# Kernel optimization log

Measured on AMD Instinct MI355X. Metric: run time of the kernel, lower is better.

## Reference

```python
import jax, jax.numpy as jnp
import numpy as np

B, S, D, H = 4, 2048, 1024, 16
DK = D // H


def setup_inputs() -> dict:
    key = jax.random.key(0)
    ks = jax.random.split(key, 12)
    def xavier(k, shape):
        fan_in, fan_out = shape[1], shape[0]
        limit = (6.0 / (fan_in + fan_out)) ** 0.5
        return jax.random.uniform(k, shape, jnp.float32, -limit, limit)
    inp = {
        "q": jax.random.normal(ks[0], (B, S, D), jnp.float32),
        "k": jax.random.normal(ks[1], (B, S, D), jnp.float32),
        "v": jax.random.normal(ks[2], (B, S, D), jnp.float32),
        "mask": jnp.ones((1, 1, S, S), jnp.int32),
        "Wq": xavier(ks[3], (D, D)), "bq": jnp.zeros((D,), jnp.float32),
        "Wk": xavier(ks[4], (D, D)), "bk": jnp.zeros((D,), jnp.float32),
        "Wv": xavier(ks[5], (D, D)), "bv": jnp.zeros((D,), jnp.float32),
        "Wo": xavier(ks[6], (D, D)), "bo": jnp.zeros((D,), jnp.float32),
        "ln_g": jnp.ones((D,), jnp.float32),
        "ln_b": jnp.zeros((D,), jnp.float32),
    }
    return inp


def _split_heads(x):
    b, s, _ = x.shape
    return x.reshape(b, s, H, DK).transpose(0, 2, 1, 3)  # [B,H,S,dk]


def reference(q, k, v, mask, Wq, bq, Wk, bk, Wv, bv, Wo, bo, ln_g, ln_b):
    residual = q
    qh = _split_heads(q @ Wq.T + bq)
    kh = _split_heads(k @ Wk.T + bk)
    vh = _split_heads(v @ Wv.T + bv)
    scale = jnp.sqrt(jnp.asarray(DK, qh.dtype))
    scores = jnp.einsum("bhqd,bhkd->bhqk", qh, kh) / scale  # [B,H,S,S]
    scores = jnp.where(mask == 0, jnp.asarray(-1e9, scores.dtype), scores)
    m = jnp.max(scores, axis=-1, keepdims=True)
    e = jnp.exp(scores - m) * mask.astype(scores.dtype)
    probs = e / (jnp.sum(e, axis=-1, keepdims=True) + 1e-9)
    attn = jnp.einsum("bhqk,bhkd->bhqd", probs, vh)
    attn = attn.transpose(0, 2, 1, 3).reshape(q.shape[0], -1, D)
    out = attn @ Wo.T + bo
    x = out + residual
    mu = jnp.mean(x, axis=-1, keepdims=True)
    var = jnp.mean((x - mu) ** 2, axis=-1, keepdims=True)
    return (x - mu) / jnp.sqrt(var + 1e-5) * ln_g + ln_b
```

## Files before the change

### kernel.cpp

```cpp
#include <hip/hip_runtime.h>
#include <hip/hip_bf16.h>
#include <stdint.h>

#define B_  4
#define S_  2048
#define D_  1024
#define H_  16
#define DK_ 64
#define M_  (B_ * S_)

typedef __bf16 bf16x8 __attribute__((ext_vector_type(8)));
typedef float  f32x4  __attribute__((ext_vector_type(4)));

__device__ __forceinline__ void gl_lds16(const void* g, void* l) {
  __builtin_amdgcn_global_load_lds(
      (const __attribute__((address_space(1))) void*)g,
      (__attribute__((address_space(3))) void*)l, 16, 0, 0);
}

__global__ __launch_bounds__(256)
void cvt_kernel(const float* __restrict__ src, __bf16* __restrict__ dst) {
  const int i = blockIdx.x * 256 + threadIdx.x;
  const float4 a = ((const float4*)src)[i * 2];
  const float4 b = ((const float4*)src)[i * 2 + 1];
  bf16x8 o;
  o[0] = (__bf16)a.x; o[1] = (__bf16)a.y; o[2] = (__bf16)a.z; o[3] = (__bf16)a.w;
  o[4] = (__bf16)b.x; o[5] = (__bf16)b.y; o[6] = (__bf16)b.z; o[7] = (__bf16)b.w;
  ((bf16x8*)dst)[i] = o;
}

__global__ __launch_bounds__(256)
void cvt_w_kernel(const float* __restrict__ s0, const float* __restrict__ s1,
                  const float* __restrict__ s2, const float* __restrict__ s3,
                  __bf16* __restrict__ dst) {
  const float* s = blockIdx.y == 0 ? s0 : blockIdx.y == 1 ? s1
                  : blockIdx.y == 2 ? s2 : s3;
  __bf16* d = dst + (long)blockIdx.y * (D_ * D_);
  const int i = blockIdx.x * 256 + threadIdx.x;
  const float4 a = ((const float4*)s)[i * 2];
  const float4 b = ((const float4*)s)[i * 2 + 1];
  bf16x8 o;
  o[0] = (__bf16)a.x; o[1] = (__bf16)a.y; o[2] = (__bf16)a.z; o[3] = (__bf16)a.w;
  o[4] = (__bf16)b.x; o[5] = (__bf16)b.y; o[6] = (__bf16)b.z; o[7] = (__bf16)b.w;
  ((bf16x8*)d)[i] = o;
}

template <int MODE>
__global__ __launch_bounds__(256)
void gemm_bt_kernel(const __bf16* __restrict__ A,
                    const __bf16* __restrict__ W,
                    const float* __restrict__ bias,
                    __bf16* __restrict__ outh,
                    float* __restrict__ outf,
                    const float* __restrict__ resid,
                    float scale) {
  __shared__ __bf16 Asm[128 * 32];
  __shared__ __bf16 Bsm[128 * 32];
  const int tid  = threadIdx.x;
  const int lane = tid & 63;
  const int wave = tid >> 6;
  const int wm = (wave >> 1) * 64, wn = (wave & 1) * 64;
  const int m0 = blockIdx.y * 128, n0 = blockIdx.x * 128;
  const int lr = lane & 15, lq = lane >> 4;

  const int r0 = tid >> 2;
  const int c0 = (tid & 3) * 8;
  const __bf16* Ap0 = A + (long)(m0 + r0) * D_ + c0;
  const __bf16* Ap1 = A + (long)(m0 + 64 + r0) * D_ + c0;
  const __bf16* Wp0 = W + (long)(n0 + r0) * D_ + c0;
  const __bf16* Wp1 = W + (long)(n0 + 64 + r0) * D_ + c0;
  __bf16* AsmW0 = &Asm[tid * 8];
  __bf16* AsmW1 = &Asm[(256 + tid) * 8];
  __bf16* BsmW0 = &Bsm[tid * 8];
  __bf16* BsmW1 = &Bsm[(256 + tid) * 8];

  f32x4 acc[4][4] = {};

  for (int k0 = 0; k0 < D_; k0 += 32) {
    gl_lds16(Ap0 + k0, AsmW0);
    gl_lds16(Ap1 + k0, AsmW1);
    gl_lds16(Wp0 + k0, BsmW0);
    gl_lds16(Wp1 + k0, BsmW1);
    __syncthreads();
    bf16x8 af[4], bf[4];
#pragma unroll
    for (int i = 0; i < 4; i++)
      af[i] = *(const bf16x8*)&Asm[(wm + i * 16 + lr) * 32 + lq * 8];
#pragma unroll
    for (int j = 0; j < 4; j++)
      bf[j] = *(const bf16x8*)&Bsm[(wn + j * 16 + lr) * 32 + lq * 8];
#pragma unroll
    for (int i = 0; i < 4; i++)
#pragma unroll
      for (int j = 0; j < 4; j++)
        acc[i][j] = __builtin_amdgcn_mfma_f32_16x16x32_bf16(af[i], bf[j],
                                                            acc[i][j], 0, 0, 0);
    __syncthreads();
  }

#pragma unroll
  for (int j = 0; j < 4; j++) {
    const int n = n0 + wn + j * 16 + lr;
    const float bb = bias[n];
#pragma unroll
    for (int i = 0; i < 4; i++) {
      const int mbase = m0 + wm + i * 16 + lq * 4;
#pragma unroll
      for (int r = 0; r < 4; r++) {
        const int m = mbase + r;
        float v = acc[i][j][r];
        if (MODE == 0) {
          v = (v + bb) * scale;
          const int b = m >> 11, s = m & (S_ - 1);
          const int h = n >> 6, dk = n & 63;
          outh[(((long)(b * H_ + h) * S_ + s)) * DK_ + dk] = (__bf16)v;
        } else {
          outf[(long)m * D_ + n] = v + bb + resid[(long)m * D_ + n];
        }
      }
    }
  }
}

__global__ __launch_bounds__(256)
void transpose_v_kernel(const __bf16* __restrict__ Vh, __bf16* __restrict__ Vt) {
  __shared__ __bf16 tile[64 * 80];
  const int tid = threadIdx.x;
  const int bh = blockIdx.y;
  const int s0 = blockIdx.x * 64;
#pragma unroll
  for (int c = 0; c < 2; c++) {
    const int idx = c * 256 + tid;
    const int sl = idx >> 3, ch = idx & 7;
    *(uint4*)&tile[sl * 80 + ch * 8] =
        *(const uint4*)&Vh[((long)bh * S_ + s0 + sl) * DK_ + ch * 8];
  }
  __syncthreads();
#pragma unroll
  for (int c = 0; c < 2; c++) {
    const int idx = c * 256 + tid;
    const int dk = idx >> 3, ch = idx & 7;
    __bf16 tmp[8];
#pragma unroll
    for (int j = 0; j < 8; j++) tmp[j] = tile[(ch * 8 + j) * 80 + dk];
    *(uint4*)&Vt[((long)bh * DK_ + dk) * S_ + s0 + ch * 8] = *(const uint4*)tmp;
  }
}

__global__ __launch_bounds__(256)
void attn_kernel(const __bf16* __restrict__ Qh,
                 const __bf16* __restrict__ Kh,
                 const __bf16* __restrict__ Vt,
                 __bf16* __restrict__ ctx) {
  __shared__ __bf16 Ksm[64 * 64];
  __shared__ __bf16 Vsm[64 * 64];
  __shared__ __bf16 Psm[4 * 32 * 72];
  const int tid = threadIdx.x, lane = tid & 63, wave = tid >> 6;
  const int lr = lane & 15, lq = lane >> 4;
  const int bh = blockIdx.z * H_ + blockIdx.y;
  const int q0 = blockIdx.x * 128 + wave * 32;
  const long base = (long)bh * S_ * DK_;
  __bf16* Pw = &Psm[wave * 32 * 72];

  bf16x8 qf[2][2];
#pragma unroll
  for (int qg = 0; qg < 2; qg++)
#pragma unroll
    for (int c = 0; c < 2; c++)
      qf[qg][c] = *(const bf16x8*)
          &Qh[base + (long)(q0 + qg * 16 + lr) * DK_ + c * 32 + lq * 8];

  f32x4 o[2][4] = {};
  float lsum[2] = {0.f, 0.f};

  for (int kt = 0; kt < S_ / 64; kt++) {
    const int k0 = kt * 64;
#pragma unroll
    for (int c = 0; c < 2; c++) {
      const int idx = c * 256 + tid;
      const int row = idx >> 3, ch = (idx & 7) * 8;
      gl_lds16(&Kh[base + (long)(k0 + row) * DK_ + ch], &Ksm[idx * 8]);
      gl_lds16(&Vt[base + (long)row * S_ + k0 + ch], &Vsm[idx * 8]);
    }
    __syncthreads();

    f32x4 sc[2][4];
#pragma unroll
    for (int nt = 0; nt < 4; nt++) {
      bf16x8 kf0 = *(const bf16x8*)&Ksm[(nt * 16 + lr) * 64 + lq * 8];
      bf16x8 kf1 = *(const bf16x8*)&Ksm[(nt * 16 + lr) * 64 + 32 + lq * 8];
#pragma unroll
      for (int qg = 0; qg < 2; qg++) {
        f32x4 z = {};
        z = __builtin_amdgcn_mfma_f32_16x16x32_bf16(kf0, qf[qg][0], z, 0, 0, 0);
        z = __builtin_amdgcn_mfma_f32_16x16x32_bf16(kf1, qf[qg][1], z, 0, 0, 0);
        sc[qg][nt] = z;
      }
    }

#pragma unroll
    for (int qg = 0; qg < 2; qg++) {
      float rs = 0.f;
      __bf16* prow = &Pw[(qg * 16 + lr) * 72 + lq * 4];
#pragma unroll
      for (int nt = 0; nt < 4; nt++) {
        union { __bf16 h[4]; uint2 u; } pk;
#pragma unroll
        for (int r = 0; r < 4; r++) {
          const float p = __builtin_amdgcn_exp2f(sc[qg][nt][r]);
          rs += p;
          pk.h[r] = (__bf16)p;
        }
        *(uint2*)&prow[nt * 16] = pk.u;
      }
      lsum[qg] += rs;
    }

    bf16x8 pf[2][2];
#pragma unroll
    for (int qg = 0; qg < 2; qg++) {
      pf[qg][0] = *(const bf16x8*)&Pw[(qg * 16 + lr) * 72 + lq * 8];
      pf[qg][1] = *(const bf16x8*)&Pw[(qg * 16 + lr) * 72 + 32 + lq * 8];
    }
#pragma unroll
    for (int d = 0; d < 4; d++) {
      bf16x8 vf0 = *(const bf16x8*)&Vsm[(d * 16 + lr) * 64 + lq * 8];
      bf16x8 vf1 = *(const bf16x8*)&Vsm[(d * 16 + lr) * 64 + 32 + lq * 8];
#pragma unroll
      for (int qg = 0; qg < 2; qg++) {
        o[qg][d] = __builtin_amdgcn_mfma_f32_16x16x32_bf16(pf[qg][0], vf0,
                                                           o[qg][d], 0, 0, 0);
        o[qg][d] = __builtin_amdgcn_mfma_f32_16x16x32_bf16(pf[qg][1], vf1,
                                                           o[qg][d], 0, 0, 0);
      }
    }
    __syncthreads();
  }

  const int b = blockIdx.z, h = blockIdx.y;
#pragma unroll
  for (int qg = 0; qg < 2; qg++) {
    float t = lsum[qg];
    t += __shfl_xor(t, 16);
    t += __shfl_xor(t, 32);
#pragma unroll
    for (int r = 0; r < 4; r++) {
      const float ls = __shfl(t, (lane & 48) | (lq * 4 + r));
      const float inv = 1.f / (ls + 1e-9f);
      const int srow = q0 + qg * 16 + lq * 4 + r;
#pragma unroll
      for (int d = 0; d < 4; d++)
        ctx[((long)b * S_ + srow) * D_ + h * DK_ + d * 16 + lr] =
            (__bf16)(o[qg][d][r] * inv);
    }
  }
}

__global__ __launch_bounds__(256)
void ln_kernel(float* __restrict__ x, const float* __restrict__ g,
               const float* __restrict__ bta) {
  const int lane = threadIdx.x & 63, wave = threadIdx.x >> 6;
  const int row = blockIdx.x * 4 + wave;
  float* xp = x + (long)row * D_;
  float v[16], sum = 0.f, ssq = 0.f;
#pragma unroll
  for (int c = 0; c < 4; c++) {
    const float4 t = *(const float4*)&xp[lane * 16 + c * 4];
    v[c * 4 + 0] = t.x; v[c * 4 + 1] = t.y; v[c * 4 + 2] = t.z; v[c * 4 + 3] = t.w;
  }
#pragma unroll
  for (int j = 0; j < 16; j++) {
    sum += v[j];
    ssq += v[j] * v[j];
  }
#pragma unroll
  for (int off = 1; off < 64; off <<= 1) {
    sum += __shfl_xor(sum, off);
    ssq += __shfl_xor(ssq, off);
  }
  const float mu = sum * (1.f / 1024.f);
  const float var = ssq * (1.f / 1024.f) - mu * mu;
  const float rstd = rsqrtf(var + 1e-5f);
#pragma unroll
  for (int c = 0; c < 4; c++) {
    float4 t;
    const int cbase = lane * 16 + c * 4;
    t.x = (v[c * 4 + 0] - mu) * rstd * g[cbase + 0] + bta[cbase + 0];
    t.y = (v[c * 4 + 1] - mu) * rstd * g[cbase + 1] + bta[cbase + 1];
    t.z = (v[c * 4 + 2] - mu) * rstd * g[cbase + 2] + bta[cbase + 2];
    t.w = (v[c * 4 + 3] - mu) * rstd * g[cbase + 3] + bta[cbase + 3];
    *(float4*)&xp[cbase] = t;
  }
}

extern "C" void kernel_launch(void* const* d_in, const int* in_sizes, int n_in,
                              void* d_out, int out_size, void* d_ws,
                              size_t ws_size, hipStream_t stream) {
  const float* q   = (const float*)d_in[0];
  const float* k   = (const float*)d_in[1];
  const float* v   = (const float*)d_in[2];
  const float* Wq  = (const float*)d_in[4];
  const float* bq  = (const float*)d_in[5];
  const float* Wk  = (const float*)d_in[6];
  const float* bk  = (const float*)d_in[7];
  const float* Wv  = (const float*)d_in[8];
  const float* bv  = (const float*)d_in[9];
  const float* Wo  = (const float*)d_in[10];
  const float* bo  = (const float*)d_in[11];
  const float* lng = (const float*)d_in[12];
  const float* lnb = (const float*)d_in[13];
  float* out = (float*)d_out;
  __bf16* ws = (__bf16*)d_ws;

  const long SZ = (long)M_ * D_;
  const long WN = (long)D_ * D_;
  __bf16* cbuf = ws;
  __bf16* Wb   = ws + SZ;
  __bf16* Qh   = ws + SZ + 4 * WN;
  __bf16* Kh   = Qh + SZ;
  __bf16* Vh   = Qh + 2 * SZ;
  __bf16* Vt   = Qh + 3 * SZ;
  __bf16* ctx  = cbuf;

  const int CG = (int)(SZ / 8 / 256);
  const dim3 gg(D_ / 128, M_ / 128);
  const float qscale = 0.125f * 1.44269504f;

  cvt_w_kernel<<<dim3(WN / 8 / 256, 4), 256, 0, stream>>>(Wq, Wk, Wv, Wo, Wb);

  cvt_kernel<<<CG, 256, 0, stream>>>(q, cbuf);
  gemm_bt_kernel<0><<<gg, 256, 0, stream>>>(cbuf, Wb + 0 * WN, bq, Qh, nullptr,
                                            nullptr, qscale);
  cvt_kernel<<<CG, 256, 0, stream>>>(k, cbuf);
  gemm_bt_kernel<0><<<gg, 256, 0, stream>>>(cbuf, Wb + 1 * WN, bk, Kh, nullptr,
                                            nullptr, 1.0f);
  cvt_kernel<<<CG, 256, 0, stream>>>(v, cbuf);
  gemm_bt_kernel<0><<<gg, 256, 0, stream>>>(cbuf, Wb + 2 * WN, bv, Vh, nullptr,
                                            nullptr, 1.0f);
  transpose_v_kernel<<<dim3(S_ / 64, B_ * H_), 256, 0, stream>>>(Vh, Vt);
  attn_kernel<<<dim3(S_ / 128, H_, B_), 256, 0, stream>>>(Qh, Kh, Vt, ctx);
  gemm_bt_kernel<1><<<gg, 256, 0, stream>>>(ctx, Wb + 3 * WN, bo, nullptr, out,
                                            q, 1.0f);
  ln_kernel<<<M_ / 4, 256, 0, stream>>>(out, lng, lnb);
}
```

Baseline: 439.1 us.

## Fuse fp32-to-bf16 conversion into batched QKV projection and swizzle LDS layouts

Removes the three separate activation conversion kernels by loading fp32 inputs directly in the projection GEMM, converting in registers and writing bf16 into LDS. The Q, K and V projections are merged into one launch using a z grid dimension. XOR swizzles are applied to the GEMM and attention LDS tiles to reduce bank conflicts. The trade-off is that A-tile loads now go through registers instead of direct global-to-LDS copies and read twice as many bytes as fp32, which may expose more load latency.

```diff
diff --git a/kernel.cpp b/kernel.cpp
--- a/kernel.cpp
+++ b/kernel.cpp
@@ -18,15 +18,11 @@
       (__attribute__((address_space(3))) void*)l, 16, 0, 0);
 }
 
-__global__ __launch_bounds__(256)
-void cvt_kernel(const float* __restrict__ src, __bf16* __restrict__ dst) {
-  const int i = blockIdx.x * 256 + threadIdx.x;
-  const float4 a = ((const float4*)src)[i * 2];
-  const float4 b = ((const float4*)src)[i * 2 + 1];
+__device__ __forceinline__ bf16x8 pack8(float4 a, float4 b) {
   bf16x8 o;
   o[0] = (__bf16)a.x; o[1] = (__bf16)a.y; o[2] = (__bf16)a.z; o[3] = (__bf16)a.w;
   o[4] = (__bf16)b.x; o[5] = (__bf16)b.y; o[6] = (__bf16)b.z; o[7] = (__bf16)b.w;
-  ((bf16x8*)dst)[i] = o;
+  return o;
 }
 
 __global__ __launch_bounds__(256)
@@ -37,23 +33,107 @@
                   : blockIdx.y == 2 ? s2 : s3;
   __bf16* d = dst + (long)blockIdx.y * (D_ * D_);
   const int i = blockIdx.x * 256 + threadIdx.x;
-  const float4 a = ((const float4*)s)[i * 2];
-  const float4 b = ((const float4*)s)[i * 2 + 1];
-  bf16x8 o;
-  o[0] = (__bf16)a.x; o[1] = (__bf16)a.y; o[2] = (__bf16)a.z; o[3] = (__bf16)a.w;
-  o[4] = (__bf16)b.x; o[5] = (__bf16)b.y; o[6] = (__bf16)b.z; o[7] = (__bf16)b.w;
-  ((bf16x8*)d)[i] = o;
-}
-
-template <int MODE>
-__global__ __launch_bounds__(256)
-void gemm_bt_kernel(const __bf16* __restrict__ A,
-                    const __bf16* __restrict__ W,
-                    const float* __restrict__ bias,
-                    __bf16* __restrict__ outh,
-                    float* __restrict__ outf,
-                    const float* __restrict__ resid,
-                    float scale) {
+  ((bf16x8*)d)[i] =
+      pack8(((const float4*)s)[i * 2], ((const float4*)s)[i * 2 + 1]);
+}
+
+__global__ __launch_bounds__(256)
+void proj_qkv_kernel(const float* __restrict__ qin, const float* __restrict__ kin,
+                     const float* __restrict__ vin, const __bf16* __restrict__ Wb,
+                     const float* __restrict__ bq, const float* __restrict__ bk,
+                     const float* __restrict__ bv, __bf16* __restrict__ Qh,
+                     float qscale) {
+  __shared__ __bf16 Asm[128 * 32];
+  __shared__ __bf16 Bsm[128 * 32];
+  const int z = blockIdx.z;
+  const float* A = z == 0 ? qin : z == 1 ? kin : vin;
+  const __bf16* W = Wb + (long)z * (D_ * D_);
+  const float* bias = z == 0 ? bq : z == 1 ? bk : bv;
+  const float scale = z == 0 ? qscale : 1.0f;
+  __bf16* dst = Qh + (long)z * ((long)M_ * D_);
+
+  const int tid  = threadIdx.x;
+  const int lane = tid & 63;
+  const int wave = tid >> 6;
+  const int wm = (wave >> 1) * 64, wn = (wave & 1) * 64;
+  const int m0 = blockIdx.y * 128, n0 = blockIdx.x * 128;
+  const int lr = lane & 15, lq = lane >> 4;
+
+  const int ar  = tid >> 1;
+  const int acg = (tid & 1) * 2;
+  const int asw = (ar >> 1) & 3;
+  const float* Aptr = A + (long)(m0 + ar) * D_ + acg * 8;
+  __bf16* AsmW0 = &Asm[ar * 32 + ((acg    ) ^ asw) * 8];
+  __bf16* AsmW1 = &Asm[ar * 32 + ((acg + 1) ^ asw) * 8];
+
+  const int r0  = tid >> 2;
+  const int bcg = ((tid & 3) ^ ((r0 >> 1) & 3)) * 8;
+  const __bf16* Wp0 = W + (long)(n0 + r0) * D_ + bcg;
+  const __bf16* Wp1 = W + (long)(n0 + 64 + r0) * D_ + bcg;
+  __bf16* BsmW0 = &Bsm[tid * 8];
+  __bf16* BsmW1 = &Bsm[(256 + tid) * 8];
+
+  int aoff[4], boff[4];
+#pragma unroll
+  for (int i = 0; i < 4; i++) {
+    const int row = wm + i * 16 + lr;
+    aoff[i] = row * 32 + ((lq ^ ((row >> 1) & 3)) * 8);
+  }
+#pragma unroll
+  for (int j = 0; j < 4; j++) {
+    const int row = wn + j * 16 + lr;
+    boff[j] = row * 32 + ((lq ^ ((row >> 1) & 3)) * 8);
+  }
+
+  f32x4 acc[4][4] = {};
+
+  for (int k0 = 0; k0 < D_; k0 += 32) {
+    const float4 f0 = *(const float4*)(Aptr + k0);
+    const float4 f1 = *(const float4*)(Aptr + k0 + 4);
+    const float4 f2 = *(const float4*)(Aptr + k0 + 8);
+    const float4 f3 = *(const float4*)(Aptr + k0 + 12);
+    gl_lds16(Wp0 + k0, BsmW0);
+    gl_lds16(Wp1 + k0, BsmW1);
+    *(bf16x8*)AsmW0 = pack8(f0, f1);
+    *(bf16x8*)AsmW1 = pack8(f2, f3);
+    __syncthreads();
+    bf16x8 af[4], bf[4];
+#pragma unroll
+    for (int i = 0; i < 4; i++) af[i] = *(const bf16x8*)&Asm[aoff[i]];
+#pragma unroll
+    for (int j = 0; j < 4; j++) bf[j] = *(const bf16x8*)&Bsm[boff[j]];
+#pragma unroll
+    for (int i = 0; i < 4; i++)
+#pragma unroll
+      for (int j = 0; j < 4; j++)
+        acc[i][j] = __builtin_amdgcn_mfma_f32_16x16x32_bf16(af[i], bf[j],
+                                                            acc[i][j], 0, 0, 0);
+    __syncthreads();
+  }
+
+#pragma unroll
+  for (int j = 0; j < 4; j++) {
+    const int n = n0 + wn + j * 16 + lr;
+    const float bb = bias[n];
+#pragma unroll
+    for (int i = 0; i < 4; i++) {
+      const int mbase = m0 + wm + i * 16 + lq * 4;
+#pragma unroll
+      for (int r = 0; r < 4; r++) {
+        const int m = mbase + r;
+        const float v = (acc[i][j][r] + bb) * scale;
+        const int b = m >> 11, s = m & (S_ - 1);
+        const int h = n >> 6, dk = n & 63;
+        dst[(((long)(b * H_ + h) * S_ + s)) * DK_ + dk] = (__bf16)v;
+      }
+    }
+  }
+}
+
+__global__ __launch_bounds__(256)
+void gemm_out_kernel(const __bf16* __restrict__ A, const __bf16* __restrict__ W,
+                     const float* __restrict__ bias, float* __restrict__ outf,
+                     const float* __restrict__ resid) {
   __shared__ __bf16 Asm[128 * 32];
   __shared__ __bf16 Bsm[128 * 32];
   const int tid  = threadIdx.x;
@@ -64,15 +144,27 @@
   const int lr = lane & 15, lq = lane >> 4;
 
   const int r0 = tid >> 2;
-  const int c0 = (tid & 3) * 8;
-  const __bf16* Ap0 = A + (long)(m0 + r0) * D_ + c0;
-  const __bf16* Ap1 = A + (long)(m0 + 64 + r0) * D_ + c0;
-  const __bf16* Wp0 = W + (long)(n0 + r0) * D_ + c0;
-  const __bf16* Wp1 = W + (long)(n0 + 64 + r0) * D_ + c0;
+  const int cg = ((tid & 3) ^ ((r0 >> 1) & 3)) * 8;
+  const __bf16* Ap0 = A + (long)(m0 + r0) * D_ + cg;
+  const __bf16* Ap1 = A + (long)(m0 + 64 + r0) * D_ + cg;
+  const __bf16* Wp0 = W + (long)(n0 + r0) * D_ + cg;
+  const __bf16* Wp1 = W + (long)(n0 + 64 + r0) * D_ + cg;
   __bf16* AsmW0 = &Asm[tid * 8];
   __bf16* AsmW1 = &Asm[(256 + tid) * 8];
   __bf16* BsmW0 = &Bsm[tid * 8];
   __bf16* BsmW1 = &Bsm[(256 + tid) * 8];
+
+  int aoff[4], boff[4];
+#pragma unroll
+  for (int i = 0; i < 4; i++) {
+    const int row = wm + i * 16 + lr;
+    aoff[i] = row * 32 + ((lq ^ ((row >> 1) & 3)) * 8);
+  }
+#pragma unroll
+  for (int j = 0; j < 4; j++) {
+    const int row = wn + j * 16 + lr;
+    boff[j] = row * 32 + ((lq ^ ((row >> 1) & 3)) * 8);
+  }
 
   f32x4 acc[4][4] = {};
 
@@ -84,11 +176,9 @@
     __syncthreads();
     bf16x8 af[4], bf[4];
 #pragma unroll
-    for (int i = 0; i < 4; i++)
-      af[i] = *(const bf16x8*)&Asm[(wm + i * 16 + lr) * 32 + lq * 8];
-#pragma unroll
-    for (int j = 0; j < 4; j++)
-      bf[j] = *(const bf16x8*)&Bsm[(wn + j * 16 + lr) * 32 + lq * 8];
+    for (int i = 0; i < 4; i++) af[i] = *(const bf16x8*)&Asm[aoff[i]];
+#pragma unroll
+    for (int j = 0; j < 4; j++) bf[j] = *(const bf16x8*)&Bsm[boff[j]];
 #pragma unroll
     for (int i = 0; i < 4; i++)
 #pragma unroll
@@ -108,15 +198,7 @@
 #pragma unroll
       for (int r = 0; r < 4; r++) {
         const int m = mbase + r;
-        float v = acc[i][j][r];
-        if (MODE == 0) {
-          v = (v + bb) * scale;
-          const int b = m >> 11, s = m & (S_ - 1);
-          const int h = n >> 6, dk = n & 63;
-          outh[(((long)(b * H_ + h) * S_ + s)) * DK_ + dk] = (__bf16)v;
-        } else {
-          outf[(long)m * D_ + n] = v + bb + resid[(long)m * D_ + n];
-        }
+        outf[(long)m * D_ + n] = acc[i][j][r] + bb + resid[(long)m * D_ + n];
       }
     }
   }
@@ -170,6 +252,10 @@
       qf[qg][c] = *(const bf16x8*)
           &Qh[base + (long)(q0 + qg * 16 + lr) * DK_ + c * 32 + lq * 8];
 
+  const int cl0 = (lq ^ (lr & 7)) * 8;
+  const int cl1 = ((lq + 4) ^ (lr & 7)) * 8;
+  const int rbase = lr * 64;
+
   f32x4 o[2][4] = {};
   float lsum[2] = {0.f, 0.f};
 
@@ -178,17 +264,18 @@
 #pragma unroll
     for (int c = 0; c < 2; c++) {
       const int idx = c * 256 + tid;
-      const int row = idx >> 3, ch = (idx & 7) * 8;
-      gl_lds16(&Kh[base + (long)(k0 + row) * DK_ + ch], &Ksm[idx * 8]);
-      gl_lds16(&Vt[base + (long)row * S_ + k0 + ch], &Vsm[idx * 8]);
+      const int row = idx >> 3;
+      const int cgl = ((idx & 7) ^ (row & 7)) * 8;
+      gl_lds16(&Kh[base + (long)(k0 + row) * DK_ + cgl], &Ksm[idx * 8]);
+      gl_lds16(&Vt[base + (long)row * S_ + k0 + cgl], &Vsm[idx * 8]);
     }
     __syncthreads();
 
     f32x4 sc[2][4];
 #pragma unroll
     for (int nt = 0; nt < 4; nt++) {
-      bf16x8 kf0 = *(const bf16x8*)&Ksm[(nt * 16 + lr) * 64 + lq * 8];
-      bf16x8 kf1 = *(const bf16x8*)&Ksm[(nt * 16 + lr) * 64 + 32 + lq * 8];
+      bf16x8 kf0 = *(const bf16x8*)&Ksm[nt * 1024 + rbase + cl0];
+      bf16x8 kf1 = *(const bf16x8*)&Ksm[nt * 1024 + rbase + cl1];
 #pragma unroll
       for (int qg = 0; qg < 2; qg++) {
         f32x4 z = {};
@@ -224,8 +311,8 @@
     }
 #pragma unroll
     for (int d = 0; d < 4; d++) {
-      bf16x8 vf0 = *(const bf16x8*)&Vsm[(d * 16 + lr) * 64 + lq * 8];
-      bf16x8 vf1 = *(const bf16x8*)&Vsm[(d * 16 + lr) * 64 + 32 + lq * 8];
+      bf16x8 vf0 = *(const bf16x8*)&Vsm[d * 1024 + rbase + cl0];
+      bf16x8 vf1 = *(const bf16x8*)&Vsm[d * 1024 + rbase + cl1];
 #pragma unroll
       for (int qg = 0; qg < 2; qg++) {
         o[qg][d] = __builtin_amdgcn_mfma_f32_16x16x32_bf16(pf[qg][0], vf0,
@@ -314,32 +401,21 @@
 
   const long SZ = (long)M_ * D_;
   const long WN = (long)D_ * D_;
-  __bf16* cbuf = ws;
-  __bf16* Wb   = ws + SZ;
-  __bf16* Qh   = ws + SZ + 4 * WN;
-  __bf16* Kh   = Qh + SZ;
-  __bf16* Vh   = Qh + 2 * SZ;
-  __bf16* Vt   = Qh + 3 * SZ;
-  __bf16* ctx  = cbuf;
-
-  const int CG = (int)(SZ / 8 / 256);
-  const dim3 gg(D_ / 128, M_ / 128);
+  __bf16* Wb  = ws;
+  __bf16* Qh  = ws + 4 * WN;
+  __bf16* Kh  = Qh + SZ;
+  __bf16* Vh  = Qh + 2 * SZ;
+  __bf16* Vt  = Qh + 3 * SZ;
+  __bf16* ctx = Vh;
+
   const float qscale = 0.125f * 1.44269504f;
 
   cvt_w_kernel<<<dim3(WN / 8 / 256, 4), 256, 0, stream>>>(Wq, Wk, Wv, Wo, Wb);
-
-  cvt_kernel<<<CG, 256, 0, stream>>>(q, cbuf);
-  gemm_bt_kernel<0><<<gg, 256, 0, stream>>>(cbuf, Wb + 0 * WN, bq, Qh, nullptr,
-                                            nullptr, qscale);
-  cvt_kernel<<<CG, 256, 0, stream>>>(k, cbuf);
-  gemm_bt_kernel<0><<<gg, 256, 0, stream>>>(cbuf, Wb + 1 * WN, bk, Kh, nullptr,
-                                            nullptr, 1.0f);
-  cvt_kernel<<<CG, 256, 0, stream>>>(v, cbuf);
-  gemm_bt_kernel<0><<<gg, 256, 0, stream>>>(cbuf, Wb + 2 * WN, bv, Vh, nullptr,
-                                            nullptr, 1.0f);
+  proj_qkv_kernel<<<dim3(D_ / 128, M_ / 128, 3), 256, 0, stream>>>(
+      q, k, v, Wb, bq, bk, bv, Qh, qscale);
   transpose_v_kernel<<<dim3(S_ / 64, B_ * H_), 256, 0, stream>>>(Vh, Vt);
   attn_kernel<<<dim3(S_ / 128, H_, B_), 256, 0, stream>>>(Qh, Kh, Vt, ctx);
-  gemm_bt_kernel<1><<<gg, 256, 0, stream>>>(ctx, Wb + 3 * WN, bo, nullptr, out,
-                                            q, 1.0f);
+  gemm_out_kernel<<<dim3(D_ / 128, M_ / 128), 256, 0, stream>>>(ctx, Wb + 3 * WN,
+                                                                bo, out, q);
   ln_kernel<<<M_ / 4, 256, 0, stream>>>(out, lng, lnb);
 }
```

Result: faster. 430.1 us (-2.1%).
